# Kernel optimization log

Hardware: AMD Instinct MI355X
Metric: run time of the kernel (lower is better)

## Reference

```python
import jax, jax.numpy as jnp
import numpy as np

B, T, I, H = 64, 512, 1024, 1024  # batch, seq_len, input_size, hidden_size


def setup_inputs() -> dict:
    key = jax.random.key(0)
    ks = jax.random.split(key, 5)
    s = 0.02
    return {
        "sequence": jax.random.normal(ks[0], (B, T, I), jnp.float32),
        "Wx0": jax.random.normal(ks[1], (4 * H, I), jnp.float32) * s,
        "Wh0": jax.random.normal(ks[2], (4 * H, H), jnp.float32) * s,
        "b0": jnp.zeros((4 * H,), jnp.float32),
        "Wx1": jax.random.normal(ks[3], (4 * H, H), jnp.float32) * s,
        "Wh1": jax.random.normal(ks[4], (4 * H, H), jnp.float32) * s,
        "b1": jnp.zeros((4 * H,), jnp.float32),
    }


def _run_layer(xs, Wx, Wh, b):
    # xs: [T, B, D_in]; packed gates order: forget, input-gate(w), candidate(i), output(m)
    batch = xs.shape[1]
    hid = Wh.shape[1]
    # precompute input projections for all timesteps: [T, B, 4H]
    xproj = jnp.einsum('tbd,gd->tbg', xs, Wx) + b

    def step(carry, xp):
        c, h = carry
        z = xp + h @ Wh.T  # [B, 4H]
        f, w, i, m = jnp.split(z, 4, axis=-1)
        c = c * jax.nn.sigmoid(f) + jax.nn.sigmoid(w) * jnp.tanh(i)
        h = jnp.tanh(c) * jax.nn.sigmoid(m)
        return (c, h), h

    init = (jnp.zeros((batch, hid), xs.dtype), jnp.zeros((batch, hid), xs.dtype))
    (c, h), hs = jax.lax.scan(step, init, xproj)
    return hs, h  # hs: [T, B, H], h: [B, H]


def reference(sequence, Wx0, Wh0, b0, Wx1, Wh1, b1):
    xs = jnp.transpose(sequence, (1, 0, 2))  # [T, B, I]
    hs0, _ = _run_layer(xs, Wx0, Wh0, b0)
    _, h_last = _run_layer(hs0, Wx1, Wh1, b1)
    return h_last  # [B, H] == H[:, :, -1] of the original
```

## Files before the change

kernel.cpp:

```cpp
#include <hip/hip_runtime.h>

typedef __bf16 bf16x8 __attribute__((ext_vector_type(8)));
typedef float f32x4 __attribute__((ext_vector_type(4)));
typedef unsigned long long u64;

__device__ inline float sigm(float x) { return 1.0f / (1.0f + __expf(-x)); }
__device__ inline float tanh_f(float x) {
    float e = __expf(2.0f * x);
    return 1.0f - 2.0f / (e + 1.0f);
}

__device__ inline unsigned short f2bf(float f) {
    __bf16 h = (__bf16)f;
    return __builtin_bit_cast(unsigned short, h);
}

__device__ inline bf16x8 cvt8(float4 lo, float4 hi) {
    bf16x8 r;
    r[0] = (__bf16)lo.x; r[1] = (__bf16)lo.y; r[2] = (__bf16)lo.z; r[3] = (__bf16)lo.w;
    r[4] = (__bf16)hi.x; r[5] = (__bf16)hi.y; r[6] = (__bf16)hi.z; r[7] = (__bf16)hi.w;
    return r;
}

__device__ inline u64 ld64c(const u64* p) {
    return __hip_atomic_load(p, __ATOMIC_RELAXED, __HIP_MEMORY_SCOPE_AGENT);
}
__device__ inline void st32c(unsigned int* p, unsigned int v) {
    __hip_atomic_store(p, v, __ATOMIC_RELAXED, __HIP_MEMORY_SCOPE_AGENT);
}
__device__ inline unsigned int ld32c(const unsigned int* p) {
    return __hip_atomic_load(p, __ATOMIC_RELAXED, __HIP_MEMORY_SCOPE_AGENT);
}


__global__ void cvt_weights(const float* __restrict__ Wx0, const float* __restrict__ Wh0,
                            const float* __restrict__ Wx1, const float* __restrict__ Wh1,
                            unsigned short* __restrict__ W0, unsigned short* __restrict__ W1) {
    size_t idx = ((size_t)blockIdx.x * 256 + threadIdx.x) * 8;
    const size_t LSZ = (size_t)4096 * 2048;
    int layer = idx >= LSZ;
    size_t e = idx - (layer ? LSZ : 0);
    int row = (int)(e >> 11);
    int k = (int)(e & 2047);
    const float* src = layer ? (k < 1024 ? Wx1 : Wh1) : (k < 1024 ? Wx0 : Wh0);
    const float* s = src + (size_t)row * 1024 + (k & 1023);
    float4 lo = ((const float4*)s)[0], hi = ((const float4*)s)[1];
    *reinterpret_cast<bf16x8*>((layer ? W1 : W0) + e) = cvt8(lo, hi);
}

__global__ void cvt_seq(const float* __restrict__ seq, unsigned short* __restrict__ seqb, int T) {
    int t = blockIdx.x >> 6, b = blockIdx.x & 63;
    int row = b & 31, btile = b >> 5, tid = threadIdx.x;
    const float* s = seq + ((size_t)b * T + t) * 1024 + tid * 8;
    float4 lo = ((const float4*)s)[0], hi = ((const float4*)s)[1];
    int off = ((row >> 4) << 14) + ((tid >> 2) << 9) + (((tid & 3) << 4) + (row & 15)) * 8;
    *reinterpret_cast<bf16x8*>(seqb + ((size_t)t * 2 + btile) * 32768 + off) = cvt8(lo, hi);
}

union SmemU {
    unsigned short a[2][32768];
    float z[4][32][16];
};

struct StageRegs { u64 q[32]; };

__device__ inline void stage_issue(StageRegs& r, const unsigned short* __restrict__ src) {
#pragma unroll
    for (int i = 0; i < 16; ++i) {
        const u64* s = (const u64*)(src + (size_t)((threadIdx.x + (i << 8)) << 3));
        r.q[2 * i] = ld64c(s);
        r.q[2 * i + 1] = ld64c(s + 1);
    }
}

__device__ inline void stage_issue_plain(StageRegs& r, const unsigned short* __restrict__ src) {
#pragma unroll
    for (int i = 0; i < 16; ++i) {
        const u64* s = (const u64*)(src + (size_t)((threadIdx.x + (i << 8)) << 3));
        r.q[2 * i] = s[0];
        r.q[2 * i + 1] = s[1];
    }
}

__device__ inline void stage_write(const StageRegs& r, unsigned short* tile) {
#pragma unroll
    for (int i = 0; i < 16; ++i) {
        u64* d = (u64*)(tile + (size_t)((threadIdx.x + (i << 8)) << 3));
        d[0] = r.q[2 * i];
        d[1] = r.q[2 * i + 1];
    }
}

template <int BASE>
__device__ inline void mfma_pass(const unsigned short* tile, const bf16x8 (&w)[64],
                                 f32x4& acc0, f32x4& acc1, int lane) {
#pragma unroll
    for (int kk = 0; kk < 32; ++kk) {
        bf16x8 av0 = *(const bf16x8*)(tile + kk * 512 + lane * 8);
        bf16x8 av1 = *(const bf16x8*)(tile + 16384 + kk * 512 + lane * 8);
        acc0 = __builtin_amdgcn_mfma_f32_16x16x32_bf16(av0, w[BASE + kk], acc0, 0, 0, 0);
        acc1 = __builtin_amdgcn_mfma_f32_16x16x32_bf16(av1, w[BASE + kk], acc1, 0, 0, 0);
    }
}

template <bool SEQB>
__global__ __launch_bounds__(256, 1) void lstm_persistent(
    const float* __restrict__ seq, const unsigned short* __restrict__ seqb,
    const unsigned short* __restrict__ W0, const unsigned short* __restrict__ W1,
    const float* __restrict__ bias0, const float* __restrict__ bias1,
    unsigned short* h0buf, unsigned short* h1buf, unsigned int* flags,
    float* out, int T) {
    const int bid = blockIdx.x;
    const int r = bid & 7, q = bid >> 3;
    const int btile = q & 1, t2 = q >> 1;
    const int layer = t2 >> 3;
    const int jtile = ((t2 & 7) << 3) | r;
    const int j0 = jtile * 16;
    const int brow = btile * 32;

    const int tid = threadIdx.x;
    const int wave = tid >> 6, lane = tid & 63;
    const int ln15 = lane & 15, lhi = lane >> 4;

    const unsigned short* Wl = layer ? W1 : W0;
    const float* bias = layer ? bias1 : bias0;
    const unsigned short* Bbase = Wl + (size_t)(wave * 1024 + j0 + ln15) * 2048 + lhi * 8;
    unsigned short* hown = layer ? h1buf : h0buf;

    __shared__ SmemU smem;

    bf16x8 wreg[64];
#pragma unroll
    for (int q2 = 0; q2 < 64; ++q2)
        wreg[q2] = *reinterpret_cast<const bf16x8*>(Bbase + q2 * 32);

    const int bl = tid >> 3;
    const int jj = (tid & 7) * 2;
    const float bf0 = bias[j0 + jj],        bf1 = bias[j0 + jj + 1];
    const float bw0 = bias[1024 + j0 + jj], bw1 = bias[1024 + j0 + jj + 1];
    const float bi0 = bias[2048 + j0 + jj], bi1 = bias[2048 + j0 + jj + 1];
    const float bm0 = bias[3072 + j0 + jj], bm1 = bias[3072 + j0 + jj + 1];
    const int colg = j0 + jj;
    const int hoff = ((bl >> 4) << 14) + ((colg >> 5) << 9) +
                     ((((colg >> 3) & 3) << 4) + (bl & 15)) * 8 + (colg & 7);

    float creg0 = 0.f, creg1 = 0.f;
    const int P = T + 2;

    for (int p = 0; p < P; ++p) {
        const bool act = layer ? (p >= 2) : (p < T);
        const int t = layer ? (p - 2) : p;
        const bool have0 = act && (layer == 1 || SEQB);

        StageRegs s0;
        if (have0) {
            if (layer == 0)
                stage_issue_plain(s0, seqb + ((size_t)t * 2 + btile) * 32768);
            else
                stage_issue(s0, h0buf + (size_t)((t % 3) * 2 + btile) * 32768);
        }

        if (p > 0) {
            const unsigned int tgt = (unsigned int)p;
            while (ld32c(&flags[tid]) < tgt) __builtin_amdgcn_s_sleep(1);
        }
        if (have0) stage_write(s0, smem.a[0]);
        __syncthreads();

        if (act) {
            f32x4 acc0 = {0.f, 0.f, 0.f, 0.f};
            f32x4 acc1 = {0.f, 0.f, 0.f, 0.f};

            StageRegs s1;
            const unsigned short* hsrc = layer
                ? h1buf + (size_t)(((t + 1) & 1) * 2 + btile) * 32768
                : h0buf + (size_t)(((t + 2) % 3) * 2 + btile) * 32768;
            stage_issue(s1, hsrc);

            if (layer == 0 && !SEQB) {
                const float* a0f = seq + ((size_t)(brow + ln15) * T + t) * 1024 + lhi * 8;
                const float* a1f = a0f + (size_t)16 * T * 1024;
#pragma unroll
                for (int kk = 0; kk < 32; ++kk) {
                    float4 l0 = ((const float4*)a0f)[0], h0v = ((const float4*)a0f)[1];
                    float4 l1 = ((const float4*)a1f)[0], h1v = ((const float4*)a1f)[1];
                    bf16x8 av0 = cvt8(l0, h0v), av1 = cvt8(l1, h1v);
                    acc0 = __builtin_amdgcn_mfma_f32_16x16x32_bf16(av0, wreg[kk], acc0, 0, 0, 0);
                    acc1 = __builtin_amdgcn_mfma_f32_16x16x32_bf16(av1, wreg[kk], acc1, 0, 0, 0);
                    a0f += 32; a1f += 32;
                }
            } else {
                mfma_pass<0>(smem.a[0], wreg, acc0, acc1, lane);
            }

            stage_write(s1, smem.a[1]);
            __syncthreads();
            mfma_pass<32>(smem.a[1], wreg, acc0, acc1, lane);

#pragma unroll
            for (int rr = 0; rr < 4; ++rr) {
                smem.z[wave][4 * lhi + rr][ln15] = acc0[rr];
                smem.z[wave][16 + 4 * lhi + rr][ln15] = acc1[rr];
            }
            __syncthreads();

            {
                float2 zf = *(const float2*)&smem.z[0][bl][jj];
                float2 zw = *(const float2*)&smem.z[1][bl][jj];
                float2 zi = *(const float2*)&smem.z[2][bl][jj];
                float2 zm = *(const float2*)&smem.z[3][bl][jj];
                float c0n = creg0 * sigm(zf.x + bf0) + sigm(zw.x + bw0) * tanh_f(zi.x + bi0);
                float c1n = creg1 * sigm(zf.y + bf1) + sigm(zw.y + bw1) * tanh_f(zi.y + bi1);
                float h0v = tanh_f(c0n) * sigm(zm.x + bm0);
                float h1v = tanh_f(c1n) * sigm(zm.y + bm1);
                creg0 = c0n; creg1 = c1n;
                const int wbuf = layer ? (t & 1) : (t % 3);
                unsigned short* tb = hown + (size_t)(wbuf * 2 + btile) * 32768;
                unsigned int packed = (unsigned int)f2bf(h0v) | ((unsigned int)f2bf(h1v) << 16);
                st32c((unsigned int*)(tb + hoff), packed);
                if (layer && t == T - 1) {
                    int idx = (brow + bl) * 1024 + colg;
                    out[idx] = h0v; out[idx + 1] = h1v;
                }
            }
        }

        if (p < P - 1) {
            __syncthreads();
            if (tid == 0) st32c(&flags[bid], (unsigned int)(p + 1));
        }
    }
}

extern "C" void kernel_launch(void* const* d_in, const int* in_sizes, int n_in,
                              void* d_out, int out_size, void* d_ws, size_t ws_size,
                              hipStream_t stream) {
    const float* seq = (const float*)d_in[0];
    const float* Wx0 = (const float*)d_in[1];
    const float* Wh0 = (const float*)d_in[2];
    const float* b0 = (const float*)d_in[3];
    const float* Wx1 = (const float*)d_in[4];
    const float* Wh1 = (const float*)d_in[5];
    const float* b1 = (const float*)d_in[6];
    float* out = (float*)d_out;
    char* ws = (char*)d_ws;
    const int T = 512;

    const size_t WBYTES = (size_t)4096 * 2048 * 2;
    const size_t SEQB_BYTES = (size_t)512 * 2 * 32768 * 2;
    const size_t H0_BYTES = 3 * 2 * 65536;
    const size_t H1_BYTES = 2 * 2 * 65536;
    const size_t STATE_BYTES = H0_BYTES + H1_BYTES + 1024;

    size_t offSeqb = 2 * WBYTES;
    bool big = ws_size >= 2 * WBYTES + SEQB_BYTES + STATE_BYTES;
    size_t offState = big ? (offSeqb + SEQB_BYTES) : offSeqb;

    unsigned short* W0p = (unsigned short*)(ws);
    unsigned short* W1p = (unsigned short*)(ws + WBYTES);
    unsigned short* seqbp = (unsigned short*)(ws + offSeqb);
    unsigned short* h0p = (unsigned short*)(ws + offState);
    unsigned short* h1p = (unsigned short*)(ws + offState + H0_BYTES);
    unsigned int* flagsp = (unsigned int*)(ws + offState + H0_BYTES + H1_BYTES);

    hipLaunchKernelGGL(cvt_weights, dim3(8192), dim3(256), 0, stream,
                       Wx0, Wh0, Wx1, Wh1, W0p, W1p);
    if (big)
        hipLaunchKernelGGL(cvt_seq, dim3(T * 64), dim3(128), 0, stream, seq, seqbp, T);
    hipMemsetAsync(ws + offState, 0, STATE_BYTES, stream);

    int Tv = T;
    void* args[] = {&seq, &seqbp, &W0p, &W1p, &b0, &b1, &h0p, &h1p, &flagsp, &out, &Tv};
    if (big) {
        hipError_t e = hipLaunchCooperativeKernel((void*)lstm_persistent<true>,
                                                  dim3(256), dim3(256), args, 0, stream);
        if (e != hipSuccess) {
            hipLaunchKernelGGL((lstm_persistent<true>), dim3(256), dim3(256), 0, stream,
                               seq, seqbp, W0p, W1p, b0, b1, h0p, h1p, flagsp, out, Tv);
        }
    } else {
        hipError_t e = hipLaunchCooperativeKernel((void*)lstm_persistent<false>,
                                                  dim3(256), dim3(256), args, 0, stream);
        if (e != hipSuccess) {
            hipLaunchKernelGGL((lstm_persistent<false>), dim3(256), dim3(256), 0, stream,
                               seq, seqbp, W0p, W1p, b0, b1, h0p, h1p, flagsp, out, Tv);
        }
    }
}
```

Before: 4.368 ms.

## Split blocks into input and recurrent wave groups pipelined one step apart

Doubles each block to 512 threads: one half computes the input projection (x or h0) for step t+1 while the other half computes the recurrent h@Wh for step t. Each thread now holds only half the weights in registers. Input-projection results are double-buffered in shared memory and the recurrent MFMA waves get raised priority. The aim is to take the input-projection GEMM off the serial recurrent critical path and drop one barrier per step. In exchange the pipeline gains a stage, more shared memory is used, the h0 ring buffer shrinks to two slots, and each thread does one element-wise output instead of two.

Result: faster. 3.744 ms (-14.3%).

```diff
diff --git a/kernel.cpp b/kernel.cpp
--- a/kernel.cpp
+++ b/kernel.cpp
@@ -30,6 +30,9 @@
 }
 __device__ inline unsigned int ld32c(const unsigned int* p) {
     return __hip_atomic_load(p, __ATOMIC_RELAXED, __HIP_MEMORY_SCOPE_AGENT);
+}
+__device__ inline void st16c(unsigned short* p, unsigned short v) {
+    __hip_atomic_store(p, v, __ATOMIC_RELAXED, __HIP_MEMORY_SCOPE_AGENT);
 }
 
 
@@ -57,54 +60,42 @@
     *reinterpret_cast<bf16x8*>(seqb + ((size_t)t * 2 + btile) * 32768 + off) = cvt8(lo, hi);
 }
 
-union SmemU {
-    unsigned short a[2][32768];
-    float z[4][32][16];
+struct Smem {
+    unsigned short ah[32768];
+    unsigned short ax[32768];
+    float zh[4][32][16];
+    float zx[2][4][32][16];
 };
 
 struct StageRegs { u64 q[32]; };
 
-__device__ inline void stage_issue(StageRegs& r, const unsigned short* __restrict__ src) {
+__device__ inline void stage_issue(StageRegs& r, const unsigned short* __restrict__ src, int ttid) {
 #pragma unroll
     for (int i = 0; i < 16; ++i) {
-        const u64* s = (const u64*)(src + (size_t)((threadIdx.x + (i << 8)) << 3));
+        const u64* s = (const u64*)(src + (size_t)((ttid + (i << 8)) << 3));
         r.q[2 * i] = ld64c(s);
         r.q[2 * i + 1] = ld64c(s + 1);
     }
 }
-
-__device__ inline void stage_issue_plain(StageRegs& r, const unsigned short* __restrict__ src) {
+__device__ inline void stage_issue_plain(StageRegs& r, const unsigned short* __restrict__ src, int ttid) {
 #pragma unroll
     for (int i = 0; i < 16; ++i) {
-        const u64* s = (const u64*)(src + (size_t)((threadIdx.x + (i << 8)) << 3));
+        const u64* s = (const u64*)(src + (size_t)((ttid + (i << 8)) << 3));
         r.q[2 * i] = s[0];
         r.q[2 * i + 1] = s[1];
     }
 }
-
-__device__ inline void stage_write(const StageRegs& r, unsigned short* tile) {
+__device__ inline void stage_write(const StageRegs& r, unsigned short* tile, int ttid) {
 #pragma unroll
     for (int i = 0; i < 16; ++i) {
-        u64* d = (u64*)(tile + (size_t)((threadIdx.x + (i << 8)) << 3));
+        u64* d = (u64*)(tile + (size_t)((ttid + (i << 8)) << 3));
         d[0] = r.q[2 * i];
         d[1] = r.q[2 * i + 1];
     }
 }
 
-template <int BASE>
-__device__ inline void mfma_pass(const unsigned short* tile, const bf16x8 (&w)[64],
-                                 f32x4& acc0, f32x4& acc1, int lane) {
-#pragma unroll
-    for (int kk = 0; kk < 32; ++kk) {
-        bf16x8 av0 = *(const bf16x8*)(tile + kk * 512 + lane * 8);
-        bf16x8 av1 = *(const bf16x8*)(tile + 16384 + kk * 512 + lane * 8);
-        acc0 = __builtin_amdgcn_mfma_f32_16x16x32_bf16(av0, w[BASE + kk], acc0, 0, 0, 0);
-        acc1 = __builtin_amdgcn_mfma_f32_16x16x32_bf16(av1, w[BASE + kk], acc1, 0, 0, 0);
-    }
-}
-
 template <bool SEQB>
-__global__ __launch_bounds__(256, 1) void lstm_persistent(
+__global__ __launch_bounds__(512, 2) void lstm_persistent(
     const float* __restrict__ seq, const unsigned short* __restrict__ seqb,
     const unsigned short* __restrict__ W0, const unsigned short* __restrict__ W1,
     const float* __restrict__ bias0, const float* __restrict__ bias1,
@@ -119,66 +110,72 @@
     const int brow = btile * 32;
 
     const int tid = threadIdx.x;
-    const int wave = tid >> 6, lane = tid & 63;
+    const int isX = tid >> 8;
+    const int ttid = tid & 255;
+    const int twave = ttid >> 6;
+    const int lane = tid & 63;
     const int ln15 = lane & 15, lhi = lane >> 4;
 
     const unsigned short* Wl = layer ? W1 : W0;
     const float* bias = layer ? bias1 : bias0;
-    const unsigned short* Bbase = Wl + (size_t)(wave * 1024 + j0 + ln15) * 2048 + lhi * 8;
     unsigned short* hown = layer ? h1buf : h0buf;
 
-    __shared__ SmemU smem;
-
-    bf16x8 wreg[64];
-#pragma unroll
-    for (int q2 = 0; q2 < 64; ++q2)
-        wreg[q2] = *reinterpret_cast<const bf16x8*>(Bbase + q2 * 32);
-
-    const int bl = tid >> 3;
-    const int jj = (tid & 7) * 2;
-    const float bf0 = bias[j0 + jj],        bf1 = bias[j0 + jj + 1];
-    const float bw0 = bias[1024 + j0 + jj], bw1 = bias[1024 + j0 + jj + 1];
-    const float bi0 = bias[2048 + j0 + jj], bi1 = bias[2048 + j0 + jj + 1];
-    const float bm0 = bias[3072 + j0 + jj], bm1 = bias[3072 + j0 + jj + 1];
+    __shared__ Smem sm;
+    unsigned short* mytile = isX ? sm.ax : sm.ah;
+
+    const unsigned short* Bb =
+        Wl + (size_t)(twave * 1024 + j0 + ln15) * 2048 + (isX ? 0 : 1024) + lhi * 8;
+    bf16x8 wreg[32];
+#pragma unroll
+    for (int k = 0; k < 32; ++k) wreg[k] = *(const bf16x8*)(Bb + k * 32);
+
+    const int bl = tid >> 4;
+    const int jj = tid & 15;
     const int colg = j0 + jj;
+    const float b_f = bias[colg], b_w = bias[1024 + colg];
+    const float b_i = bias[2048 + colg], b_m = bias[3072 + colg];
     const int hoff = ((bl >> 4) << 14) + ((colg >> 5) << 9) +
                      ((((colg >> 3) & 3) << 4) + (bl & 15)) * 8 + (colg & 7);
-
-    float creg0 = 0.f, creg1 = 0.f;
-    const int P = T + 2;
-
+    float creg = 0.f;
+
+    const int P = T + 3;
     for (int p = 0; p < P; ++p) {
-        const bool act = layer ? (p >= 2) : (p < T);
-        const int t = layer ? (p - 2) : p;
-        const bool have0 = act && (layer == 1 || SEQB);
-
-        StageRegs s0;
-        if (have0) {
-            if (layer == 0)
-                stage_issue_plain(s0, seqb + ((size_t)t * 2 + btile) * 32768);
-            else
-                stage_issue(s0, h0buf + (size_t)((t % 3) * 2 + btile) * 32768);
-        }
-
-        if (p > 0) {
+        const int tx = layer ? (p - 2) : p;
+        const int th = layer ? (p - 3) : (p - 1);
+        const bool actx = (tx >= 0) && (tx < T);
+        const bool acth = (th >= 0) && (th < T);
+        const bool myact = isX ? actx : acth;
+
+        if (p > 0 && myact && !(isX && layer == 0)) {
             const unsigned int tgt = (unsigned int)p;
-            while (ld32c(&flags[tid]) < tgt) __builtin_amdgcn_s_sleep(1);
-        }
-        if (have0) stage_write(s0, smem.a[0]);
+            const unsigned int* f = &flags[(isX ? 0 : layer * 128) + (tid & 127)];
+            while (ld32c(f) < tgt) __builtin_amdgcn_s_sleep(1);
+        }
+
+        if (myact) {
+            StageRegs s;
+            if (isX) {
+                if (layer == 0) {
+                    if (SEQB) {
+                        stage_issue_plain(s, seqb + ((size_t)tx * 2 + btile) * 32768, ttid);
+                        stage_write(s, sm.ax, ttid);
+                    }
+                } else {
+                    stage_issue(s, h0buf + (size_t)((tx & 1) * 2 + btile) * 32768, ttid);
+                    stage_write(s, sm.ax, ttid);
+                }
+            } else {
+                stage_issue(s, hown + (size_t)(((th - 1) & 1) * 2 + btile) * 32768, ttid);
+                stage_write(s, sm.ah, ttid);
+            }
+        }
         __syncthreads();
 
-        if (act) {
+        if (myact) {
             f32x4 acc0 = {0.f, 0.f, 0.f, 0.f};
             f32x4 acc1 = {0.f, 0.f, 0.f, 0.f};
-
-            StageRegs s1;
-            const unsigned short* hsrc = layer
-                ? h1buf + (size_t)(((t + 1) & 1) * 2 + btile) * 32768
-                : h0buf + (size_t)(((t + 2) % 3) * 2 + btile) * 32768;
-            stage_issue(s1, hsrc);
-
-            if (layer == 0 && !SEQB) {
-                const float* a0f = seq + ((size_t)(brow + ln15) * T + t) * 1024 + lhi * 8;
+            if (isX && layer == 0 && !SEQB) {
+                const float* a0f = seq + ((size_t)(brow + ln15) * T + tx) * 1024 + lhi * 8;
                 const float* a1f = a0f + (size_t)16 * T * 1024;
 #pragma unroll
                 for (int kk = 0; kk < 32; ++kk) {
@@ -190,39 +187,38 @@
                     a0f += 32; a1f += 32;
                 }
             } else {
-                mfma_pass<0>(smem.a[0], wreg, acc0, acc1, lane);
+                const unsigned short* tile = mytile;
+                if (!isX) __builtin_amdgcn_s_setprio(1);
+#pragma unroll
+                for (int kk = 0; kk < 32; ++kk) {
+                    bf16x8 av0 = *(const bf16x8*)(tile + kk * 512 + lane * 8);
+                    bf16x8 av1 = *(const bf16x8*)(tile + 16384 + kk * 512 + lane * 8);
+                    acc0 = __builtin_amdgcn_mfma_f32_16x16x32_bf16(av0, wreg[kk], acc0, 0, 0, 0);
+                    acc1 = __builtin_amdgcn_mfma_f32_16x16x32_bf16(av1, wreg[kk], acc1, 0, 0, 0);
+                }
+                if (!isX) __builtin_amdgcn_s_setprio(0);
             }
-
-            stage_write(s1, smem.a[1]);
-            __syncthreads();
-            mfma_pass<32>(smem.a[1], wreg, acc0, acc1, lane);
-
+            float* zd = isX ? &sm.zx[tx & 1][twave][0][0] : &sm.zh[twave][0][0];
 #pragma unroll
             for (int rr = 0; rr < 4; ++rr) {
-                smem.z[wave][4 * lhi + rr][ln15] = acc0[rr];
-                smem.z[wave][16 + 4 * lhi + rr][ln15] = acc1[rr];
+                zd[(4 * lhi + rr) * 16 + ln15] = acc0[rr];
+                zd[(16 + 4 * lhi + rr) * 16 + ln15] = acc1[rr];
             }
-            __syncthreads();
-
-            {
-                float2 zf = *(const float2*)&smem.z[0][bl][jj];
-                float2 zw = *(const float2*)&smem.z[1][bl][jj];
-                float2 zi = *(const float2*)&smem.z[2][bl][jj];
-                float2 zm = *(const float2*)&smem.z[3][bl][jj];
-                float c0n = creg0 * sigm(zf.x + bf0) + sigm(zw.x + bw0) * tanh_f(zi.x + bi0);
-                float c1n = creg1 * sigm(zf.y + bf1) + sigm(zw.y + bw1) * tanh_f(zi.y + bi1);
-                float h0v = tanh_f(c0n) * sigm(zm.x + bm0);
-                float h1v = tanh_f(c1n) * sigm(zm.y + bm1);
-                creg0 = c0n; creg1 = c1n;
-                const int wbuf = layer ? (t & 1) : (t % 3);
-                unsigned short* tb = hown + (size_t)(wbuf * 2 + btile) * 32768;
-                unsigned int packed = (unsigned int)f2bf(h0v) | ((unsigned int)f2bf(h1v) << 16);
-                st32c((unsigned int*)(tb + hoff), packed);
-                if (layer && t == T - 1) {
-                    int idx = (brow + bl) * 1024 + colg;
-                    out[idx] = h0v; out[idx + 1] = h1v;
-                }
-            }
+        }
+        __syncthreads();
+
+        if (acth) {
+            const int zb = th & 1;
+            float zf = sm.zh[0][bl][jj] + sm.zx[zb][0][bl][jj] + b_f;
+            float zw = sm.zh[1][bl][jj] + sm.zx[zb][1][bl][jj] + b_w;
+            float zi = sm.zh[2][bl][jj] + sm.zx[zb][2][bl][jj] + b_i;
+            float zm = sm.zh[3][bl][jj] + sm.zx[zb][3][bl][jj] + b_m;
+            float cn = creg * sigm(zf) + sigm(zw) * tanh_f(zi);
+            float h = tanh_f(cn) * sigm(zm);
+            creg = cn;
+            unsigned short* tb = hown + (size_t)((th & 1) * 2 + btile) * 32768;
+            st16c(tb + hoff, f2bf(h));
+            if (layer && th == T - 1) out[(brow + bl) * 1024 + colg] = h;
         }
 
         if (p < P - 1) {
@@ -248,7 +244,7 @@
 
     const size_t WBYTES = (size_t)4096 * 2048 * 2;
     const size_t SEQB_BYTES = (size_t)512 * 2 * 32768 * 2;
-    const size_t H0_BYTES = 3 * 2 * 65536;
+    const size_t H0_BYTES = 2 * 2 * 65536;
     const size_t H1_BYTES = 2 * 2 * 65536;
     const size_t STATE_BYTES = H0_BYTES + H1_BYTES + 1024;
 
@@ -273,16 +269,16 @@
     void* args[] = {&seq, &seqbp, &W0p, &W1p, &b0, &b1, &h0p, &h1p, &flagsp, &out, &Tv};
     if (big) {
         hipError_t e = hipLaunchCooperativeKernel((void*)lstm_persistent<true>,
-                                                  dim3(256), dim3(256), args, 0, stream);
+                                                  dim3(256), dim3(512), args, 0, stream);
         if (e != hipSuccess) {
-            hipLaunchKernelGGL((lstm_persistent<true>), dim3(256), dim3(256), 0, stream,
+            hipLaunchKernelGGL((lstm_persistent<true>), dim3(256), dim3(512), 0, stream,
                                seq, seqbp, W0p, W1p, b0, b1, h0p, h1p, flagsp, out, Tv);
         }
     } else {
         hipError_t e = hipLaunchCooperativeKernel((void*)lstm_persistent<false>,
-                                                  dim3(256), dim3(256), args, 0, stream);
+                                                  dim3(256), dim3(512), args, 0, stream);
         if (e != hipSuccess) {
-            hipLaunchKernelGGL((lstm_persistent<false>), dim3(256), dim3(256), 0, stream,
+            hipLaunchKernelGGL((lstm_persistent<false>), dim3(256), dim3(512), 0, stream,
                                seq, seqbp, W0p, W1p, b0, b1, h0p, h1p, flagsp, out, Tv);
         }
     }
```
